# Performance work log

Hardware: AMD Instinct MI355X
Metric: run time of the kernel (lower is better)

## Reference

```python
import jax, jax.numpy as jnp
from jax import lax
import numpy as np

B, L, N_NODES, EMB, TDIM, H, NCLS = 512, 200, 100000, 128, 10, 256, 2
IN = TDIM + EMB  # 138


def setup_inputs() -> dict:
    key = jax.random.key(0)
    ks = jax.random.split(key, 16)
    x = jax.random.randint(ks[0], (B, L, 2), 0, N_NODES, dtype=jnp.int64)
    s = 0.05
    inp = {
        'x': x,
        'emb_table': jax.random.normal(ks[1], (N_NODES, EMB), jnp.float32) * s,
        'ts_W': jnp.ones((1, TDIM), jnp.float32),
        'w_ih_f': jax.random.normal(ks[2], (4 * H, IN), jnp.float32) * s,
        'w_hh_f': jax.random.normal(ks[3], (4 * H, H), jnp.float32) * s,
        'b_ih_f': jax.random.normal(ks[4], (4 * H,), jnp.float32) * s,
        'b_hh_f': jax.random.normal(ks[5], (4 * H,), jnp.float32) * s,
        'w_ih_b': jax.random.normal(ks[6], (4 * H, IN), jnp.float32) * s,
        'w_hh_b': jax.random.normal(ks[7], (4 * H, H), jnp.float32) * s,
        'b_ih_b': jax.random.normal(ks[8], (4 * H,), jnp.float32) * s,
        'b_hh_b': jax.random.normal(ks[9], (4 * H,), jnp.float32) * s,
        'fc_W': jax.random.normal(ks[10], (NCLS, 2 * H), jnp.float32) * s,
        'fc_b': jax.random.normal(ks[11], (NCLS,), jnp.float32) * s,
    }
    return inp


def _lstm_dir(x_seq, w_ih, w_hh, b_ih, b_hh, reverse):
    # x_seq: [B, L, F]; PyTorch gate order i, f, g, o
    bsz = x_seq.shape[0]
    h_dim = w_hh.shape[1]
    xg = jnp.einsum('blf,gf->blg', x_seq, w_ih) + b_ih + b_hh  # [B, L, 4H]
    xs = jnp.swapaxes(xg, 0, 1)  # [L, B, 4H]
    if reverse:
        xs = xs[::-1]

    def step(carry, xg_t):
        h, c = carry
        g = xg_t + h @ w_hh.T
        i, f, gg, o = jnp.split(g, 4, axis=-1)
        c = jax.nn.sigmoid(f) * c + jax.nn.sigmoid(i) * jnp.tanh(gg)
        h = jax.nn.sigmoid(o) * jnp.tanh(c)
        return (h, c), h

    z = jnp.zeros((bsz, h_dim), x_seq.dtype)
    _, hs = lax.scan(step, (z, z), xs)
    hs = jnp.swapaxes(hs, 0, 1)  # [B, L, H]
    if reverse:
        hs = hs[:, ::-1]
    return hs


def reference(x, emb_table, ts_W, w_ih_f, w_hh_f, b_ih_f, b_hh_f,
              w_ih_b, w_hh_b, b_ih_b, b_hh_b, fc_W, fc_b):
    # timestamp embedding: [B, L, 1] @ [1, 10] -> [B, L, 10]
    t = x[:, :, 0:1].astype(jnp.float32)
    t_emb = t @ ts_W
    # F.normalize(p=2, dim=1): L2-normalize over the sequence axis
    norm = jnp.sqrt(jnp.sum(t_emb * t_emb, axis=1, keepdims=True))
    t_emb = t_emb / jnp.maximum(norm, 1e-12)

    # vectorized node-embedding gather; id == -1 -> zero vector
    ids = x[:, :, 1]
    gathered = emb_table[jnp.clip(ids, 0, None)]  # [B, L, 128]
    l_emb = jnp.where((ids >= 0)[..., None], gathered, jnp.zeros((), gathered.dtype))

    embedding = jnp.concatenate([t_emb, l_emb], axis=2)  # [B, L, 138]

    h_f = _lstm_dir(embedding, w_ih_f, w_hh_f, b_ih_f, b_hh_f, reverse=False)
    h_b = _lstm_dir(embedding, w_ih_b, w_hh_b, b_ih_b, b_hh_b, reverse=True)
    out = jnp.concatenate([h_f, h_b], axis=-1)  # [B, L, 2H]

    return out[:, -1, :] @ fc_W.T + fc_b  # [B, num_classes]
```

## Files before the change

kernel.cpp:

```cpp
#include <hip/hip_runtime.h>
#include <stdint.h>


typedef unsigned short u16;
typedef __bf16 bf16x8 __attribute__((ext_vector_type(8)));
typedef float  f32x4  __attribute__((ext_vector_type(4)));
typedef float  f32x2  __attribute__((ext_vector_type(2)));
typedef int    i32x4v __attribute__((ext_vector_type(4)));
typedef int    i32x8v __attribute__((ext_vector_type(8)));

#define B_    512
#define L_    200
#define EMB_  128
#define TDIM_ 10
#define IN_   138
#define INP_  160
#define H_    256
#define G4_   1024
#define T_    200
#define DS_   (1.0f/1024.0f)
#define LOG2E 1.4426950408889634f
#define EXP2(x) __builtin_amdgcn_exp2f(x)
#define RCP(x)  __builtin_amdgcn_rcpf(x)

static __device__ __forceinline__ float bf2f(u16 u) {
  union { uint32_t i; float f; } v; v.i = ((uint32_t)u) << 16; return v.f;
}
static __device__ __forceinline__ u16 f2bf(float f) {
  __bf16 h = (__bf16)f; return __builtin_bit_cast(u16, h);
}
static __device__ __forceinline__ float bflo(uint32_t u) {
  return __builtin_bit_cast(float, (uint32_t)(u << 16));
}
static __device__ __forceinline__ float bfhi(uint32_t u) {
  return __builtin_bit_cast(float, (uint32_t)(u & 0xffff0000u));
}
static __device__ __forceinline__ float sigf(float x) {
  return RCP(1.0f + EXP2(-x * LOG2E));
}
static __device__ __forceinline__ float tanh_(float x) {
  x = fminf(fmaxf(x, -15.f), 15.f);
  float e = EXP2(2.0f * LOG2E * x);
  return (e - 1.0f) * RCP(e + 1.0f);
}
static __device__ __forceinline__ f32x4 mfma16(bf16x8 a, bf16x8 b, f32x4 c) {
  return __builtin_amdgcn_mfma_f32_16x16x32_bf16(a, b, c, 0, 0, 0);
}
static __device__ __forceinline__ f32x4 vzero4() {
  f32x4 v; v[0] = 0.f; v[1] = 0.f; v[2] = 0.f; v[3] = 0.f; return v;
}

__global__ void k_prep_mx(const float* __restrict__ whh, int* __restrict__ wf8) {
  int idx = blockIdx.x * blockDim.x + threadIdx.x;
  int d = idx & 7;
  int lane = (idx >> 3) & 63;
  int fs = idx >> 9;
  int kp2 = fs & 1, tt = (fs >> 1) & 7, w = fs >> 4;
  int mm = lane & 15, q = lane >> 4;
  int g = (w + 8 * tt) * 16 + mm;
  int k = kp2 * 128 + q * 32 + d * 4;
  const float* src = whh + g * 256 + k;
  int v = __builtin_amdgcn_cvt_pk_fp8_f32(src[0] * 64.f, src[1] * 64.f, 0, false);
  v     = __builtin_amdgcn_cvt_pk_fp8_f32(src[2] * 64.f, src[3] * 64.f, v, true);
  wf8[idx] = v;
}

__global__ __launch_bounds__(256) void k_feat(
    const int* __restrict__ x, const float* __restrict__ emb,
    const float* __restrict__ tsW, u16* __restrict__ feat) {
  __shared__ float sh_t[224];
  __shared__ int   sh_id[224];
  __shared__ float sh_s[4];
  const int b = blockIdx.x, tid = threadIdx.x;
  float v = 0.f;
  if (tid < L_) {
    int2 p = *(const int2*)&x[(b * L_ + tid) * 2];
    float t = (float)p.x;
    sh_t[tid] = t;
    sh_id[tid] = p.y;
    v = t * t;
  }
  #pragma unroll
  for (int o = 32; o; o >>= 1) v += __shfl_down(v, o);
  if ((tid & 63) == 0) sh_s[tid >> 6] = v;
  __syncthreads();
  const float sq = sqrtf(sh_s[0] + sh_s[1] + sh_s[2] + sh_s[3]);
  for (int i = tid; i < L_ * INP_; i += 256) {
    int l = i / INP_, c = i - l * INP_;
    float v2 = 0.f;
    if (c < TDIM_) {
      float wd = tsW[c];
      float den = fmaxf(fabsf(wd) * sq, 1e-12f);
      v2 = sh_t[l] * wd * RCP(den);
    } else if (c < IN_) {
      int id = sh_id[l];
      float e = emb[(long)(id < 0 ? 0 : id) * EMB_ + (c - TDIM_)];
      v2 = (id >= 0) ? e : 0.f;
    }
    feat[(long)b * (L_ * INP_) + i] = f2bf(v2);
  }
}

__global__ __launch_bounds__(512, 2) void k_xg(
    const u16* __restrict__ feat, const float* __restrict__ wih,
    const float* __restrict__ bih, const float* __restrict__ bhh,
    u16* __restrict__ xg) {
  __shared__ u16 Bs[256 * 176];
  const int nt = blockIdx.x;
  const int mt = blockIdx.y;
  const int tid = threadIdx.x;
  const int w = tid >> 6, lane = tid & 63;
  const int q = lane >> 4, nm = lane & 15;
  for (int i2 = tid; i2 < 256 * 88; i2 += 512) {
    int gl = i2 / 88, f2 = (i2 % 88) * 2;
    int pk = 0;
    if (f2 < IN_) {
      float2 v = *(const float2*)(wih + (long)(nt * 256 + gl) * IN_ + f2);
      pk = (int)f2bf(v.x) | ((int)f2bf(v.y) << 16);
    }
    *(int*)&Bs[gl * 176 + f2] = pk;
  }
  float bias[16];
  #pragma unroll
  for (int nu = 0; nu < 16; ++nu) {
    int g = nt * 256 + nu * 16 + nm;
    bias[nu] = bih[g] + bhh[g];
  }
  __syncthreads();
  f32x4 acc[2][16];
  #pragma unroll
  for (int m = 0; m < 2; ++m)
    #pragma unroll
    for (int nu = 0; nu < 16; ++nu) acc[m][nu] = vzero4();
  const u16* arow = feat + (long)(mt * 256 + w * 32) * INP_;
  #pragma unroll
  for (int kp = 0; kp < 5; ++kp) {
    bf16x8 a0 = *(const bf16x8*)(arow + (nm * INP_ + kp * 32 + q * 8));
    bf16x8 a1 = *(const bf16x8*)(arow + ((16 + nm) * INP_ + kp * 32 + q * 8));
    #pragma unroll
    for (int nu = 0; nu < 16; ++nu) {
      bf16x8 bb = *(const bf16x8*)&Bs[(nu * 16 + nm) * 176 + kp * 32 + q * 8];
      acc[0][nu] = mfma16(a0, bb, acc[0][nu]);
      acc[1][nu] = mfma16(a1, bb, acc[1][nu]);
    }
  }
  u16* Os = Bs;
  #pragma unroll
  for (int p = 0; p < 2; ++p) {
    __syncthreads();
    if ((w >> 2) == p) {
      #pragma unroll
      for (int nu = 0; nu < 16; ++nu)
        #pragma unroll
        for (int m = 0; m < 2; ++m)
          #pragma unroll
          for (int r = 0; r < 4; ++r) {
            int row = (w & 3) * 32 + m * 16 + 4 * q + r;
            Os[row * 264 + nu * 16 + nm] = f2bf((acc[m][nu][r] + bias[nu]) * 1024.f);
          }
    }
    __syncthreads();
    #pragma unroll
    for (int it = 0; it < 8; ++it) {
      int flat = it * 512 + tid;
      int row = flat >> 5, c = flat & 31;
      uint4 v = *(const uint4*)&Os[row * 264 + c * 8];
      *(uint4*)&xg[(long)(mt * 256 + p * 128 + row) * G4_ + nt * 256 + c * 8] = v;
    }
  }
}

#define F8MA(accv, Aa, Bv) \
  asm volatile("v_mfma_f32_16x16x128_f8f6f4 %0, %1, %2, %0" \
               : "+v"(accv) : "a"(Aa), "v"(Bv));
#define AINIT(i) \
  f32x4 acc##i; acc##i[0] = bflo(pf##i.x); acc##i[1] = bfhi(pf##i.x); \
  acc##i[2] = bflo(pf##i.y); acc##i[3] = bfhi(pf##i.y);
#define PFL(i, ptr) pf##i = *(const uint2*)((ptr) + (16 * (w + 16 * (i)) + 4 * q));
#define EPI(ai, af, ag, ao, cs2, hv2) f32x2 hv2; { \
  f32x2 xi = (ai) * c_sig, xf = (af) * c_sig, xo = (ao) * c_sig, xgv = (ag) * c_tg; \
  f32x2 ei, ef, eo, eg, ec; \
  ei[0] = EXP2(xi[0]); ei[1] = EXP2(xi[1]); \
  ef[0] = EXP2(xf[0]); ef[1] = EXP2(xf[1]); \
  eo[0] = EXP2(xo[0]); eo[1] = EXP2(xo[1]); \
  eg[0] = EXP2(xgv[0]); eg[1] = EXP2(xgv[1]); \
  f32x2 t1 = ef + 1.f; \
  f32x2 r1; r1[0] = RCP(t1[0]); r1[1] = RCP(t1[1]); \
  f32x2 t2 = (ei + 1.f) * (eg + 1.f); \
  f32x2 r2; r2[0] = RCP(t2[0]); r2[1] = RCP(t2[1]); \
  f32x2 c = cs2 * r1 + (eg - 1.f) * r2; \
  cs2 = c; \
  f32x2 xc = c * c_tc; \
  ec[0] = EXP2(xc[0]); ec[1] = EXP2(xc[1]); \
  f32x2 t3 = (eo + 1.f) * (ec + 1.f); \
  f32x2 r3; r3[0] = RCP(t3[0]); r3[1] = RCP(t3[1]); \
  hv2 = (ec * 16.f - 16.f) * r3; }

#define FSOLD(M, kp2) (((M) & 7) * 16 + ((M) >> 3) * 2 + (kp2))
#define WLOAD(M, kp2) (*(const i32x8v*)(wf8 + ((long)(FSOLD(M, kp2)) * 64 + lane) * 8))

__global__ __launch_bounds__(1024, 4) void k_lstm_f(
    const int* __restrict__ wf8, const u16* __restrict__ xg,
    float* __restrict__ hf,
    const u16* __restrict__ feat, const float* __restrict__ wihb,
    const float* __restrict__ bihb, const float* __restrict__ bhhb,
    float* __restrict__ hb) {
  __shared__ int hls[2][8 * 68];

  if (blockIdx.x >= 64) {
    const int b0 = (blockIdx.x - 64) * 8;
    const int tid = threadIdx.x;
    float* fv = (float*)hls;
    __shared__ float fv2[32];
    (void)fv2;
    for (int i = tid; i < 8 * IN_; i += 1024) {
      int r = i / IN_, c = i - r * IN_;
      fv[r * IN_ + c] = bf2f(feat[((long)(b0 + r) * L_ + (L_ - 1)) * INP_ + c]);
    }
    __syncthreads();
    const int col = tid & 255, rq = tid >> 8;
    float gi0 = bihb[col] + bhhb[col];
    float gg0 = bihb[512 + col] + bhhb[512 + col];
    float go0 = bihb[768 + col] + bhhb[768 + col];
    float gi1 = gi0, gg1 = gg0, go1 = go0;
    const float* wi_ = wihb + (long)col * IN_;
    const float* wg_ = wihb + (long)(512 + col) * IN_;
    const float* wo_ = wihb + (long)(768 + col) * IN_;
    const float* f0 = fv + (rq * 2) * IN_;
    const float* f1 = fv + (rq * 2 + 1) * IN_;
    for (int f = 0; f < IN_; ++f) {
      float a = wi_[f], g = wg_[f], o = wo_[f];
      float x0 = f0[f], x1 = f1[f];
      gi0 += a * x0; gi1 += a * x1;
      gg0 += g * x0; gg1 += g * x1;
      go0 += o * x0; go1 += o * x1;
    }
    float c0 = sigf(gi0) * tanh_(gg0);
    float c1 = sigf(gi1) * tanh_(gg1);
    hb[(long)(b0 + rq * 2) * H_ + col]     = sigf(go0) * tanh_(c0);
    hb[(long)(b0 + rq * 2 + 1) * H_ + col] = sigf(go1) * tanh_(c1);
    return;
  }

  const int tid = threadIdx.x;
  const int w = tid >> 6;
  const int lane = tid & 63;
  const int q = lane >> 4;
  const int nn = lane & 15;
  const int sl = nn & 7;
  const int hi = (nn >> 3) & 1;
  const int b = blockIdx.x * 8 + sl;
  const float c_sig = -DS_ * LOG2E;
  const float c_tg  = 2.f * DS_ * LOG2E;
  const float c_tc  = 2.f * LOG2E;

  i32x8v A00 = WLOAD(w, 0),      A01 = WLOAD(w, 1);
  i32x8v A10 = WLOAD(w + 16, 0), A11 = WLOAD(w + 16, 1);
  i32x8v A20 = WLOAD(w + 32, 0), A21 = WLOAD(w + 32, 1);
  i32x8v A30 = WLOAD(w + 48, 0), A31 = WLOAD(w + 48, 1);
  for (int i = tid; i < 8 * 68; i += 1024) hls[0][i] = 0;

  const u16* xgb = xg + (long)b * (L_ * G4_);
  uint2 pf0, pf1, pf2, pf3;
  PFL(0, xgb) PFL(1, xgb) PFL(2, xgb) PFL(3, xgb)
  f32x2 cs; cs[0] = 0.f; cs[1] = 0.f;
  __syncthreads();

  #pragma unroll 1
  for (int t = 0; t < T_; ++t) {
    const int* hr = hls[t & 1];
    i32x8v B0 = *(const i32x8v*)&hr[sl * 68 + q * 8];
    i32x8v B1 = *(const i32x8v*)&hr[sl * 68 + 32 + q * 8];
    AINIT(0) AINIT(1) AINIT(2) AINIT(3)
    {
      const u16* xn = xgb + (long)(t + 1 < T_ ? t + 1 : t) * G4_;
      PFL(0, xn) PFL(1, xn) PFL(2, xn) PFL(3, xn)
    }
    F8MA(acc0, A00, B0) F8MA(acc1, A10, B0) F8MA(acc2, A20, B0) F8MA(acc3, A30, B0)
    F8MA(acc0, A01, B1) F8MA(acc1, A11, B1) F8MA(acc2, A21, B1) F8MA(acc3, A31, B1)
    asm volatile("s_nop 7\n\ts_nop 7"
                 : "+v"(acc0), "+v"(acc1), "+v"(acc2), "+v"(acc3));
    int* hw = hls[1 - (t & 1)];
    f32x2 ai; ai[0] = hi ? acc0[2] : acc0[0]; ai[1] = hi ? acc0[3] : acc0[1];
    f32x2 af; af[0] = hi ? acc1[2] : acc1[0]; af[1] = hi ? acc1[3] : acc1[1];
    f32x2 ag; ag[0] = hi ? acc2[2] : acc2[0]; ag[1] = hi ? acc2[3] : acc2[1];
    f32x2 ao; ao[0] = hi ? acc3[2] : acc3[0]; ao[1] = hi ? acc3[3] : acc3[1];
    EPI(ai, af, ag, ao, cs, hv)
    int pk = __builtin_amdgcn_cvt_pk_fp8_f32(hv[0], hv[1], 0, false);
    ((unsigned short*)hw)[sl * 136 + 8 * w + 2 * q + hi] = (unsigned short)pk;
    if (t == T_ - 1) {
      f32x2 ov; ov[0] = hv[0] * 0.0625f; ov[1] = hv[1] * 0.0625f;
      *(f32x2*)&hf[(long)b * H_ + 16 * w + 4 * q + 2 * hi] = ov;
    }
    __asm__ volatile("" ::: "memory");
    __builtin_amdgcn_s_waitcnt(0xc07f);
    __builtin_amdgcn_s_barrier();
    __asm__ volatile("" ::: "memory");
  }
}

__global__ void k_fc(const float* __restrict__ hf, const float* __restrict__ hb,
                     const float* __restrict__ fcw, const float* __restrict__ fcb,
                     float* __restrict__ out) {
  int b = blockIdx.x;
  int lane = threadIdx.x;
  float p0 = 0.f, p1 = 0.f;
  #pragma unroll
  for (int k = lane; k < 2 * H_; k += 64) {
    float v = (k < H_) ? hf[b * H_ + k] : hb[b * H_ + (k - H_)];
    p0 += v * fcw[k];
    p1 += v * fcw[2 * H_ + k];
  }
  #pragma unroll
  for (int o = 32; o; o >>= 1) {
    p0 += __shfl_down(p0, o);
    p1 += __shfl_down(p1, o);
  }
  if (lane == 0) {
    out[b * 2 + 0] = p0 + fcb[0];
    out[b * 2 + 1] = p1 + fcb[1];
  }
}

extern "C" void kernel_launch(void* const* d_in, const int* in_sizes, int n_in,
                              void* d_out, int out_size, void* d_ws, size_t ws_size,
                              hipStream_t stream) {
  const int*   x    = (const int*)  d_in[0];
  const float* emb  = (const float*)d_in[1];
  const float* tsW  = (const float*)d_in[2];
  const float* wihf = (const float*)d_in[3];
  const float* whhf = (const float*)d_in[4];
  const float* bihf = (const float*)d_in[5];
  const float* bhhf = (const float*)d_in[6];
  const float* wihb = (const float*)d_in[7];
  const float* bihb = (const float*)d_in[9];
  const float* bhhb = (const float*)d_in[10];
  const float* fcw  = (const float*)d_in[11];
  const float* fcb  = (const float*)d_in[12];
  float* out = (float*)d_out;

  char* ws = (char*)d_ws;
  int*   wf8  = (int*)  (ws + 2048);
  u16*   feat = (u16*)  (ws + 264192);
  u16*   xg   = (u16*)  (ws + 33032192);
  float* hf   = (float*)(ws + 242747392);
  float* hb   = (float*)(ws + 243271680);

  k_prep_mx<<<dim3(256),    dim3(256),  0, stream>>>(whhf, wf8);
  k_feat   <<<dim3(512),    dim3(256),  0, stream>>>(x, emb, tsW, feat);
  k_xg     <<<dim3(4, 400), dim3(512),  0, stream>>>(feat, wihf, bihf, bhhf, xg);
  k_lstm_f <<<dim3(128),    dim3(1024), 0, stream>>>(wf8, xg, hf,
                                                     feat, wihb, bihb, bhhb, hb);
  k_fc     <<<dim3(512),    dim3(64),   0, stream>>>(hf, hb, fcw, fcb, out);
}
```

Baseline: 729.7 us.

## Split recurrent LSTM blocks to four batch rows with eight waves each

Reworks the forward-recurrence kernel so each block handles 4 batch rows with 512 threads instead of 8 rows with 1024, doubling the grid. Each wave now holds 8 M-tiles of recurrent weights and issues 16 FP8 MFMAs per step, and the MFMA output columns are remapped to 4 batches × 4 column positions. The epilogue selects one of four accumulator lanes, and the new h is written to LDS as single fp8 bytes instead of packed pairs. The intent is to spread the latency-bound recurrence over more CUs and make each block barrier cheaper. In exchange it doubles per-wave register state and serial MFMA work, and the backward-direction helper blocks shrink to match.

```diff
diff --git a/kernel.cpp b/kernel.cpp
--- a/kernel.cpp
+++ b/kernel.cpp
@@ -173,10 +173,7 @@
 #define F8MA(accv, Aa, Bv) \
   asm volatile("v_mfma_f32_16x16x128_f8f6f4 %0, %1, %2, %0" \
                : "+v"(accv) : "a"(Aa), "v"(Bv));
-#define AINIT(i) \
-  f32x4 acc##i; acc##i[0] = bflo(pf##i.x); acc##i[1] = bfhi(pf##i.x); \
-  acc##i[2] = bflo(pf##i.y); acc##i[3] = bfhi(pf##i.y);
-#define PFL(i, ptr) pf##i = *(const uint2*)((ptr) + (16 * (w + 16 * (i)) + 4 * q));
+
 #define EPI(ai, af, ag, ao, cs2, hv2) f32x2 hv2; { \
   f32x2 xi = (ai) * c_sig, xf = (af) * c_sig, xo = (ao) * c_sig, xgv = (ag) * c_tg; \
   f32x2 ei, ef, eo, eg, ec; \
@@ -199,23 +196,21 @@
 #define FSOLD(M, kp2) (((M) & 7) * 16 + ((M) >> 3) * 2 + (kp2))
 #define WLOAD(M, kp2) (*(const i32x8v*)(wf8 + ((long)(FSOLD(M, kp2)) * 64 + lane) * 8))
 
-__global__ __launch_bounds__(1024, 4) void k_lstm_f(
+__global__ __launch_bounds__(512, 2) void k_lstm_f(
     const int* __restrict__ wf8, const u16* __restrict__ xg,
     float* __restrict__ hf,
     const u16* __restrict__ feat, const float* __restrict__ wihb,
     const float* __restrict__ bihb, const float* __restrict__ bhhb,
     float* __restrict__ hb) {
-  __shared__ int hls[2][8 * 68];
-
-  if (blockIdx.x >= 64) {
-    const int b0 = (blockIdx.x - 64) * 8;
+  __shared__ int hls[2][4 * 68];
+  __shared__ float fvb[560];
+
+  if (blockIdx.x >= 128) {
+    const int b0 = (blockIdx.x - 128) * 4;
     const int tid = threadIdx.x;
-    float* fv = (float*)hls;
-    __shared__ float fv2[32];
-    (void)fv2;
-    for (int i = tid; i < 8 * IN_; i += 1024) {
+    for (int i = tid; i < 4 * IN_; i += 512) {
       int r = i / IN_, c = i - r * IN_;
-      fv[r * IN_ + c] = bf2f(feat[((long)(b0 + r) * L_ + (L_ - 1)) * INP_ + c]);
+      fvb[r * IN_ + c] = bf2f(feat[((long)(b0 + r) * L_ + (L_ - 1)) * INP_ + c]);
     }
     __syncthreads();
     const int col = tid & 255, rq = tid >> 8;
@@ -226,8 +221,8 @@
     const float* wi_ = wihb + (long)col * IN_;
     const float* wg_ = wihb + (long)(512 + col) * IN_;
     const float* wo_ = wihb + (long)(768 + col) * IN_;
-    const float* f0 = fv + (rq * 2) * IN_;
-    const float* f1 = fv + (rq * 2 + 1) * IN_;
+    const float* f0 = fvb + (rq * 2) * IN_;
+    const float* f1 = fvb + (rq * 2 + 1) * IN_;
     for (int f = 0; f < IN_; ++f) {
       float a = wi_[f], g = wg_[f], o = wo_[f];
       float x0 = f0[f], x1 = f1[f];
@@ -247,50 +242,71 @@
   const int lane = tid & 63;
   const int q = lane >> 4;
   const int nn = lane & 15;
-  const int sl = nn & 7;
-  const int hi = (nn >> 3) & 1;
-  const int b = blockIdx.x * 8 + sl;
+  const int sl = nn & 3;
+  const int cp = nn >> 2;
+  const bool c1 = (cp & 1) != 0, c2 = (cp & 2) != 0;
+  const int b = blockIdx.x * 4 + sl;
+  const int r0 = 16 * w + 4 * q + cp;
   const float c_sig = -DS_ * LOG2E;
   const float c_tg  = 2.f * DS_ * LOG2E;
   const float c_tc  = 2.f * LOG2E;
 
-  i32x8v A00 = WLOAD(w, 0),      A01 = WLOAD(w, 1);
-  i32x8v A10 = WLOAD(w + 16, 0), A11 = WLOAD(w + 16, 1);
-  i32x8v A20 = WLOAD(w + 32, 0), A21 = WLOAD(w + 32, 1);
-  i32x8v A30 = WLOAD(w + 48, 0), A31 = WLOAD(w + 48, 1);
-  for (int i = tid; i < 8 * 68; i += 1024) hls[0][i] = 0;
+  i32x8v A[8][2];
+  #pragma unroll
+  for (int j = 0; j < 8; ++j) {
+    A[j][0] = WLOAD(w + 8 * j, 0);
+    A[j][1] = WLOAD(w + 8 * j, 1);
+  }
+  for (int i = tid; i < 4 * 68; i += 512) hls[0][i] = 0;
 
   const u16* xgb = xg + (long)b * (L_ * G4_);
-  uint2 pf0, pf1, pf2, pf3;
-  PFL(0, xgb) PFL(1, xgb) PFL(2, xgb) PFL(3, xgb)
+  uint2 pf[8];
+  #pragma unroll
+  for (int j = 0; j < 8; ++j)
+    pf[j] = *(const uint2*)(xgb + (16 * (w + 8 * j) + 4 * q));
   f32x2 cs; cs[0] = 0.f; cs[1] = 0.f;
   __syncthreads();
 
   #pragma unroll 1
   for (int t = 0; t < T_; ++t) {
-    const int* hr = hls[t & 1];
-    i32x8v B0 = *(const i32x8v*)&hr[sl * 68 + q * 8];
-    i32x8v B1 = *(const i32x8v*)&hr[sl * 68 + 32 + q * 8];
-    AINIT(0) AINIT(1) AINIT(2) AINIT(3)
+    const char* hr = (const char*)hls[t & 1];
+    i32x8v B0 = *(const i32x8v*)(hr + sl * 272 + q * 32);
+    i32x8v B1 = *(const i32x8v*)(hr + sl * 272 + 128 + q * 32);
+    f32x4 acc[8];
+    #pragma unroll
+    for (int j = 0; j < 8; ++j) {
+      acc[j][0] = bflo(pf[j].x); acc[j][1] = bfhi(pf[j].x);
+      acc[j][2] = bflo(pf[j].y); acc[j][3] = bfhi(pf[j].y);
+    }
     {
       const u16* xn = xgb + (long)(t + 1 < T_ ? t + 1 : t) * G4_;
-      PFL(0, xn) PFL(1, xn) PFL(2, xn) PFL(3, xn)
-    }
-    F8MA(acc0, A00, B0) F8MA(acc1, A10, B0) F8MA(acc2, A20, B0) F8MA(acc3, A30, B0)
-    F8MA(acc0, A01, B1) F8MA(acc1, A11, B1) F8MA(acc2, A21, B1) F8MA(acc3, A31, B1)
+      #pragma unroll
+      for (int j = 0; j < 8; ++j)
+        pf[j] = *(const uint2*)(xn + (16 * (w + 8 * j) + 4 * q));
+    }
+    #pragma unroll
+    for (int j = 0; j < 8; ++j) { F8MA(acc[j], A[j][0], B0) }
+    #pragma unroll
+    for (int j = 0; j < 8; ++j) { F8MA(acc[j], A[j][1], B1) }
     asm volatile("s_nop 7\n\ts_nop 7"
-                 : "+v"(acc0), "+v"(acc1), "+v"(acc2), "+v"(acc3));
-    int* hw = hls[1 - (t & 1)];
-    f32x2 ai; ai[0] = hi ? acc0[2] : acc0[0]; ai[1] = hi ? acc0[3] : acc0[1];
-    f32x2 af; af[0] = hi ? acc1[2] : acc1[0]; af[1] = hi ? acc1[3] : acc1[1];
-    f32x2 ag; ag[0] = hi ? acc2[2] : acc2[0]; ag[1] = hi ? acc2[3] : acc2[1];
-    f32x2 ao; ao[0] = hi ? acc3[2] : acc3[0]; ao[1] = hi ? acc3[3] : acc3[1];
+                 : "+v"(acc[0]), "+v"(acc[1]), "+v"(acc[2]), "+v"(acc[3]),
+                   "+v"(acc[4]), "+v"(acc[5]), "+v"(acc[6]), "+v"(acc[7]));
+    char* hw = (char*)hls[1 - (t & 1)];
+    f32x2 ai; ai[0] = c2 ? (c1 ? acc[0][3] : acc[0][2]) : (c1 ? acc[0][1] : acc[0][0]);
+              ai[1] = c2 ? (c1 ? acc[1][3] : acc[1][2]) : (c1 ? acc[1][1] : acc[1][0]);
+    f32x2 af; af[0] = c2 ? (c1 ? acc[2][3] : acc[2][2]) : (c1 ? acc[2][1] : acc[2][0]);
+              af[1] = c2 ? (c1 ? acc[3][3] : acc[3][2]) : (c1 ? acc[3][1] : acc[3][0]);
+    f32x2 ag; ag[0] = c2 ? (c1 ? acc[4][3] : acc[4][2]) : (c1 ? acc[4][1] : acc[4][0]);
+              ag[1] = c2 ? (c1 ? acc[5][3] : acc[5][2]) : (c1 ? acc[5][1] : acc[5][0]);
+    f32x2 ao; ao[0] = c2 ? (c1 ? acc[6][3] : acc[6][2]) : (c1 ? acc[6][1] : acc[6][0]);
+              ao[1] = c2 ? (c1 ? acc[7][3] : acc[7][2]) : (c1 ? acc[7][1] : acc[7][0]);
     EPI(ai, af, ag, ao, cs, hv)
     int pk = __builtin_amdgcn_cvt_pk_fp8_f32(hv[0], hv[1], 0, false);
-    ((unsigned short*)hw)[sl * 136 + 8 * w + 2 * q + hi] = (unsigned short)pk;
+    hw[sl * 272 + r0]       = (char)pk;
+    hw[sl * 272 + 128 + r0] = (char)(pk >> 8);
     if (t == T_ - 1) {
-      f32x2 ov; ov[0] = hv[0] * 0.0625f; ov[1] = hv[1] * 0.0625f;
-      *(f32x2*)&hf[(long)b * H_ + 16 * w + 4 * q + 2 * hi] = ov;
+      hf[(long)b * H_ + r0]       = hv[0] * 0.0625f;
+      hf[(long)b * H_ + 128 + r0] = hv[1] * 0.0625f;
     }
     __asm__ volatile("" ::: "memory");
     __builtin_amdgcn_s_waitcnt(0xc07f);
@@ -349,7 +365,7 @@
   k_prep_mx<<<dim3(256),    dim3(256),  0, stream>>>(whhf, wf8);
   k_feat   <<<dim3(512),    dim3(256),  0, stream>>>(x, emb, tsW, feat);
   k_xg     <<<dim3(4, 400), dim3(512),  0, stream>>>(feat, wihf, bihf, bhhf, xg);
-  k_lstm_f <<<dim3(128),    dim3(1024), 0, stream>>>(wf8, xg, hf,
+  k_lstm_f <<<dim3(256),    dim3(512),  0, stream>>>(wf8, xg, hf,
                                                      feat, wihb, bihb, bhhb, hb);
   k_fc     <<<dim3(512),    dim3(64),   0, stream>>>(hf, hb, fcw, fcb, out);
 }
```

Result: no change. 727.8 us (-0.3%).
